# Kernel optimization log

Measured on AMD Instinct MI355X. Metric: run time of the kernel, lower is better.

The kernel has to match this reference:

```python
import jax, jax.numpy as jnp
import numpy as np

K_HOPS = 10
ALPHA = 0.1


def setup_inputs() -> dict:
    key = jax.random.key(0)
    ks = jax.random.split(key, 12)
    B, H, N, IC, F, C = 4096, 5, 30, 256, 512, 4
    real = jax.random.normal(ks[0], (B, N, IC), jnp.float32)
    imag = jax.random.normal(ks[1], (B, N, IC), jnp.float32)
    graph = jax.random.normal(ks[2], (B, H, N, N), jnp.float32)
    def lin(k, fan_in, shape):
        s = 1.0 / np.sqrt(fan_in)
        return jax.random.uniform(k, shape, jnp.float32, -s, s)
    W1 = lin(ks[3], IC, (IC, F)); b1 = lin(ks[4], IC, (F,))
    W2 = lin(ks[5], F, (F, F));  b2 = lin(ks[6], F, (F,))
    Wl = lin(ks[7], F, (F, 1));  bl = lin(ks[8], F, (1,))
    Wc = lin(ks[9], N, (C, N));  bc = lin(ks[10], N, (C,))
    return {"real": real, "imag": imag, "graph": graph,
            "W1": W1, "b1": b1, "W2": W2, "b2": b2,
            "Wl": Wl, "bl": bl, "Wc": Wc, "bc": bc}


def _appnp(S, x):
    # x_{k+1} = alpha * x0 + (1 - alpha) * S @ x_k, K iterations
    x0 = x
    def step(h, _):
        h = ALPHA * x0 + (1.0 - ALPHA) * jnp.einsum('bij,bjf->bif', S, h)
        return h, None
    h, _ = jax.lax.scan(step, x, None, length=K_HOPS)
    return h


def _prop_matrix(graph):
    # adj = mean over frequency dim; edges = nonzero entries (weights discarded
    # by the original code), self loops added, symmetric gcn_norm with
    # degree = column sums; source->target flow => operator is transposed.
    adj = jnp.mean(graph, axis=1)                      # [B,N,N]
    M = (adj != 0).astype(graph.dtype)
    N = M.shape[-1]
    Mt = M + jnp.eye(N, dtype=graph.dtype)             # add self loops
    deg = jnp.sum(Mt, axis=-2)                         # in-degree (col sums) [B,N]
    dinv = jax.lax.rsqrt(deg)
    S = dinv[:, :, None] * jnp.swapaxes(Mt, -1, -2) * dinv[:, None, :]
    return S


def reference(real, imag, graph, W1, b1, W2, b2, Wl, bl, Wc, bc):
    S = _prop_matrix(graph)
    # layer 1: linear -> relu -> APPNP(K=10)
    x = jax.nn.relu(jnp.einsum('bni,if->bnf', real, W1) + b1)
    x = _appnp(S, x)
    # layer 2: linear -> relu -> APPNP(K=10)
    x = jax.nn.relu(jnp.einsum('bnf,fg->bng', x, W2) + b2)
    x = _appnp(S, x)
    # readout: per-node linear to scalar, relu, then Conv1d(30->C, k=1)
    x = jax.nn.relu(jnp.einsum('bnf,fo->bno', x, Wl)[..., 0] + bl[0])  # [B,N]
    out = jnp.einsum('bn,cn->bc', x, Wc) + bc                          # [B,C]
    return out
```

## Files before the change

kernel.cpp:

```cpp
#include <hip/hip_runtime.h>
#include <hip/hip_bf16.h>

typedef _Float16 f16;
typedef _Float16 f16x8 __attribute__((ext_vector_type(8)));
typedef _Float16 f16x4 __attribute__((ext_vector_type(4)));
typedef float f32x4 __attribute__((ext_vector_type(4)));

#define P_OFF   0
#define W1T_OFF 14745600
#define W2T_OFF 15007744

__global__ __launch_bounds__(256) void k_prop(const float* __restrict__ graph,
                                              float* __restrict__ P,
                                              const float* __restrict__ W1,
                                              const float* __restrict__ W2,
                                              f16* __restrict__ w1t,
                                              f16* __restrict__ w2t) {
    __shared__ float MtS[4][990];
    __shared__ float dinvS[4][32];
    __shared__ f16 qhS[4][1024];
    __shared__ f16 qlS[4][1024];

    if (blockIdx.x >= 1024) {
        long base = ((long)(blockIdx.x - 1024) * 256 + threadIdx.x) * 8;
        #pragma unroll
        for (int j = 0; j < 8; ++j) {
            long id = base + j;
            if (id < 131072) {
                int f = (int)(id >> 8), k = (int)(id & 255);
                w1t[id] = (f16)W1[k * 512 + f];
            } else {
                long i = id - 131072;
                int f = (int)(i >> 9), k = (int)(i & 511);
                w2t[i] = (f16)W2[k * 512 + f];
            }
        }
        return;
    }

    const int wv = threadIdx.x >> 6, lane = threadIdx.x & 63;
    const int lr = lane & 15, gq = lane >> 4;
    const long b = (long)blockIdx.x * 4 + wv;
    const float* g = graph + b * 4500;
    float* Mt = MtS[wv];
    float* dinv = dinvS[wv];
    f16* qh = qhS[wv];
    f16* ql = qlS[wv];

    for (int rep = 0; rep < 15; ++rep) {
        int e = rep * 64 + lane;
        if (e < 900) {
            float s = g[e] + g[900 + e] + g[1800 + e] + g[2700 + e] + g[3600 + e];
            int r = e / 30, c = e - r * 30;
            Mt[r * 33 + c] = ((s != 0.f) ? 1.f : 0.f) + ((r == c) ? 1.f : 0.f);
        }
    }
    __syncthreads();
    if (lane < 30) {
        float d = 0.f;
        #pragma unroll
        for (int r = 0; r < 30; ++r) d += Mt[r * 33 + lane];
        dinv[lane] = 1.0f / sqrtf(d);
    }
    __syncthreads();

    auto Sval = [&](int i, int j) -> float {
        if (i >= 30 || j >= 30) return 0.f;
        return dinv[i] * Mt[j * 33 + i] * dinv[j];
    };

    f16x8 sh[2], sl[2];
    #pragma unroll
    for (int mi = 0; mi < 2; ++mi)
        #pragma unroll
        for (int jj = 0; jj < 8; ++jj) {
            float v = Sval(mi * 16 + lr, gq * 8 + jj);
            f16 h = (f16)v;
            sh[mi][jj] = h;
            sl[mi][jj] = (f16)(v - (float)h);
        }

    f32x4 qd[2][2], racc[2][2];
    #pragma unroll
    for (int mi = 0; mi < 2; ++mi)
        #pragma unroll
        for (int ni = 0; ni < 2; ++ni)
            #pragma unroll
            for (int r = 0; r < 4; ++r) {
                int row = mi * 16 + gq * 4 + r, col = ni * 16 + lr;
                qd[mi][ni][r] = Sval(row, col);
                racc[mi][ni][r] = (row == col) ? 0.1f : 0.f;
            }

    float c = 0.1f;
    for (int k = 1; k <= 9; ++k) {
        c *= 0.9f;
        #pragma unroll
        for (int mi = 0; mi < 2; ++mi)
            #pragma unroll
            for (int ni = 0; ni < 2; ++ni) {
                racc[mi][ni] += c * qd[mi][ni];
                f16x4 hh, ll;
                #pragma unroll
                for (int r = 0; r < 4; ++r) {
                    float v = qd[mi][ni][r];
                    f16 h = (f16)v;
                    hh[r] = h;
                    ll[r] = (f16)(v - (float)h);
                }
                const int col = ni * 16 + lr, rowb = mi * 16 + gq * 4;
                *reinterpret_cast<f16x4*>(qh + col * 32 + rowb) = hh;
                *reinterpret_cast<f16x4*>(ql + col * 32 + rowb) = ll;
            }
        __syncthreads();
        f16x8 bh[2], bl[2];
        #pragma unroll
        for (int ni = 0; ni < 2; ++ni) {
            const int col = ni * 16 + lr;
            bh[ni] = *reinterpret_cast<const f16x8*>(qh + col * 32 + gq * 8);
            bl[ni] = *reinterpret_cast<const f16x8*>(ql + col * 32 + gq * 8);
        }
        #pragma unroll
        for (int mi = 0; mi < 2; ++mi)
            #pragma unroll
            for (int ni = 0; ni < 2; ++ni) {
                f32x4 d = {0.f, 0.f, 0.f, 0.f};
                d = __builtin_amdgcn_mfma_f32_16x16x32_f16(sh[mi], bh[ni], d, 0, 0, 0);
                d = __builtin_amdgcn_mfma_f32_16x16x32_f16(sh[mi], bl[ni], d, 0, 0, 0);
                d = __builtin_amdgcn_mfma_f32_16x16x32_f16(sl[mi], bh[ni], d, 0, 0, 0);
                qd[mi][ni] = d;
            }
        __syncthreads();
    }
    const float cf = 0.3486784401f;
    #pragma unroll
    for (int mi = 0; mi < 2; ++mi)
        #pragma unroll
        for (int ni = 0; ni < 2; ++ni)
            #pragma unroll
            for (int r = 0; r < 4; ++r) {
                int row = mi * 16 + gq * 4 + r, col = ni * 16 + lr;
                if (row < 30 && col < 30)
                    P[b * 900 + row * 30 + col] = racc[mi][ni][r] + cf * qd[mi][ni][r];
            }
}

#define SMEM_BYTES 152576
#define PF_OFF   131072
#define B1L_OFF  141312
#define B2L_OFF  143360
#define WLL_OFF  145408
#define RED_OFF  147456
#define VL_OFF   151552
#define ZL_OFF   152064

__global__ __launch_bounds__(512, 2) void k_main(
    const float* __restrict__ real, const f16* __restrict__ w1t,
    const f16* __restrict__ w2t, const float* __restrict__ b1,
    const float* __restrict__ b2, const float* __restrict__ wl,
    const float* __restrict__ bl, const float* __restrict__ wc,
    const float* __restrict__ bc, const float* __restrict__ Pws,
    float* __restrict__ out) {
    extern __shared__ char smem[];
    char*  buf = smem;
    f16*   Pf  = (f16*)(smem + PF_OFF);
    float* b1l = (float*)(smem + B1L_OFF);
    float* b2l = (float*)(smem + B2L_OFF);
    float* wll = (float*)(smem + WLL_OFF);
    float* red = (float*)(smem + RED_OFF);
    float* vl  = (float*)(smem + VL_OFF);
    float* zl  = (float*)(smem + ZL_OFF);

    const int tid  = threadIdx.x;
    const int lane = tid & 63;
    const int wv   = tid >> 6;
    const int gq   = lane >> 4;
    const int lr   = lane & 15;
    const int blk  = blockIdx.x;
    const long r0  = (long)blk * 120;

    {
        const int srow = tid >> 2;
        const int seg  = tid & 3;
        const int rr   = srow & 31;
        const bool valid = rr < 30;
        const float* p = real + (r0 + (long)(srow >> 5) * 30 + rr) * 256 + seg * 64;
        #pragma unroll
        for (int q = 0; q < 8; ++q) {
            f32x4 v0 = {0.f,0.f,0.f,0.f}, v1 = {0.f,0.f,0.f,0.f};
            if (valid) {
                v0 = *reinterpret_cast<const f32x4*>(p + q * 8);
                v1 = *reinterpret_cast<const f32x4*>(p + q * 8 + 4);
            }
            f16x8 h;
            h[0]=(f16)v0[0]; h[1]=(f16)v0[1]; h[2]=(f16)v0[2]; h[3]=(f16)v0[3];
            h[4]=(f16)v1[0]; h[5]=(f16)v1[1]; h[6]=(f16)v1[2]; h[7]=(f16)v1[3];
            *reinterpret_cast<f16x8*>(
                buf + srow * 512 + ((seg * 128 + q * 16) ^ ((srow & 7) << 4))) = h;
        }
    }
    #pragma unroll
    for (int s = 0; s < 8; ++s) {
        int e = tid + s * 512;
        int bb = e >> 10, idx = e & 1023, n = idx >> 5, kk = idx & 31;
        float p = (n < 30 && kk < 30)
            ? Pws[((long)blk * 4 + bb) * 900 + n * 30 + kk] : 0.f;
        Pf[bb * 1280 + n * 40 + kk] = (f16)p;
    }
    b1l[tid] = b1[tid];
    b2l[tid] = b2[tid];
    wll[tid] = wl[tid];

    f32x4 acc[4][8];
    #pragma unroll
    for (int a = 0; a < 4; ++a)
        #pragma unroll
        for (int b = 0; b < 8; ++b) { f32x4 z = {0.f,0.f,0.f,0.f}; acc[a][b] = z; }
    __syncthreads();

    const f16* w1p = w1t + (wv * 64 + lr) * 256;
    {
        f16x8 waA[4], waB[4];
        #pragma unroll
        for (int mi = 0; mi < 4; ++mi) {
            waA[mi] = *reinterpret_cast<const f16x8*>(w1p + mi * 4096 + gq * 8);
            waB[mi] = *reinterpret_cast<const f16x8*>(w1p + mi * 4096 + 32 + gq * 8);
        }
        #pragma unroll
        for (int kc2 = 0; kc2 < 4; ++kc2) {
            #pragma unroll
            for (int half = 0; half < 2; ++half) {
                const int kc = 2 * kc2 + half;
                f16x8 bf[8];
                #pragma unroll
                for (int ni = 0; ni < 8; ++ni) {
                    const int row = ni * 16 + lr;
                    bf[ni] = *reinterpret_cast<const f16x8*>(
                        buf + row * 512 + ((kc * 64 + gq * 16) ^ ((row & 7) << 4)));
                }
                __builtin_amdgcn_s_setprio(1);
                #pragma unroll
                for (int mi = 0; mi < 4; ++mi)
                    #pragma unroll
                    for (int ni = 0; ni < 8; ++ni)
                        acc[mi][ni] = __builtin_amdgcn_mfma_f32_16x16x32_f16(
                            half ? waB[mi] : waA[mi], bf[ni], acc[mi][ni], 0, 0, 0);
                __builtin_amdgcn_s_setprio(0);
                if (kc + 2 < 8) {
                    #pragma unroll
                    for (int mi = 0; mi < 4; ++mi) {
                        f16x8 w = *reinterpret_cast<const f16x8*>(
                            w1p + mi * 4096 + (kc + 2) * 32 + gq * 8);
                        if (half) waB[mi] = w; else waA[mi] = w;
                    }
                }
            }
        }
    }
    __syncthreads();

    #pragma unroll
    for (int mi = 0; mi < 4; ++mi) {
        const int featb = wv * 64 + mi * 16 + gq * 4;
        float b1v[4];
        #pragma unroll
        for (int j = 0; j < 4; ++j) b1v[j] = b1l[featb + j];
        #pragma unroll
        for (int ni = 0; ni < 8; ++ni) {
            const int node = ni * 16 + lr;
            f16x4 h;
            #pragma unroll
            for (int j = 0; j < 4; ++j)
                h[j] = (f16)fmaxf(acc[mi][ni][j] + b1v[j], 0.f);
            *reinterpret_cast<f16x4*>(
                buf + node * 1024 + ((featb * 2) ^ ((node & 15) << 4))) = h;
        }
    }
    #pragma unroll
    for (int a = 0; a < 4; ++a)
        #pragma unroll
        for (int b = 0; b < 8; ++b) { f32x4 z = {0.f,0.f,0.f,0.f}; acc[a][b] = z; }
    __syncthreads();

    const f16* w2p = w2t + (wv * 64 + lr) * 512;
    {
        f16x8 bfA[4], bfB[4];
        #pragma unroll
        for (int ni = 0; ni < 4; ++ni) {
            bfA[ni] = *reinterpret_cast<const f16x8*>(w2p + ni * 8192 + gq * 8);
            bfB[ni] = *reinterpret_cast<const f16x8*>(w2p + ni * 8192 + 32 + gq * 8);
        }
        #pragma unroll
        for (int kc2 = 0; kc2 < 8; ++kc2) {
            #pragma unroll
            for (int half = 0; half < 2; ++half) {
                const int kc = 2 * kc2 + half;
                f16x8 af[8];
                #pragma unroll
                for (int mi = 0; mi < 8; ++mi) {
                    const int row = mi * 16 + lr;
                    af[mi] = *reinterpret_cast<const f16x8*>(
                        buf + row * 1024 + (((kc * 32 + gq * 8) * 2) ^ ((row & 15) << 4)));
                }
                __builtin_amdgcn_s_setprio(1);
                #pragma unroll
                for (int mi = 0; mi < 8; ++mi)
                    #pragma unroll
                    for (int ni = 0; ni < 4; ++ni)
                        acc[ni][mi] = __builtin_amdgcn_mfma_f32_16x16x32_f16(
                            af[mi], half ? bfB[ni] : bfA[ni], acc[ni][mi], 0, 0, 0);
                __builtin_amdgcn_s_setprio(0);
                if (kc + 2 < 16) {
                    #pragma unroll
                    for (int ni = 0; ni < 4; ++ni) {
                        f16x8 w = *reinterpret_cast<const f16x8*>(
                            w2p + ni * 8192 + (kc + 2) * 32 + gq * 8);
                        if (half) bfB[ni] = w; else bfA[ni] = w;
                    }
                }
            }
        }
    }
    __syncthreads();

    #pragma unroll
    for (int mi = 0; mi < 8; ++mi)
        #pragma unroll
        for (int ni = 0; ni < 4; ++ni) {
            const int feat  = wv * 64 + ni * 16 + lr;
            const int node0 = mi * 16 + gq * 4;
            f16x4 h;
            #pragma unroll
            for (int j = 0; j < 4; ++j) h[j] = (f16)acc[ni][mi][j];
            *reinterpret_cast<f16x4*>(
                buf + feat * 256 + ((node0 * 2) ^ ((feat & 15) << 4))) = h;
        }
    __syncthreads();

    {
        f16x8 pb[4][2];
        #pragma unroll
        for (int bb = 0; bb < 4; ++bb)
            #pragma unroll
            for (int ni = 0; ni < 2; ++ni)
                pb[bb][ni] = *reinterpret_cast<const f16x8*>(
                    Pf + bb * 1280 + (ni * 16 + lr) * 40 + gq * 8);
        float vacc[4][2];
        #pragma unroll
        for (int bb = 0; bb < 4; ++bb)
            #pragma unroll
            for (int ni = 0; ni < 2; ++ni) vacc[bb][ni] = 0.f;
        #pragma unroll
        for (int mi = 0; mi < 4; ++mi) {
            const int featb = wv * 64 + mi * 16;
            float b2v[4], wlv[4];
            #pragma unroll
            for (int j = 0; j < 4; ++j) {
                b2v[j] = b2l[featb + gq * 4 + j];
                wlv[j] = wll[featb + gq * 4 + j];
            }
            f16x8 au[4];
            #pragma unroll
            for (int bb = 0; bb < 4; ++bb) {
                const int feat = featb + lr;
                au[bb] = *reinterpret_cast<const f16x8*>(
                    buf + feat * 256 + ((bb * 64 + gq * 16) ^ ((feat & 15) << 4)));
            }
            #pragma unroll
            for (int bb = 0; bb < 4; ++bb)
                #pragma unroll
                for (int ni = 0; ni < 2; ++ni) {
                    f32x4 d = {0.f,0.f,0.f,0.f};
                    d = __builtin_amdgcn_mfma_f32_16x16x32_f16(au[bb], pb[bb][ni], d, 0, 0, 0);
                    #pragma unroll
                    for (int j = 0; j < 4; ++j) {
                        float y = fmaxf(d[j] + b2v[j], 0.f);
                        vacc[bb][ni] = fmaf(y, wlv[j], vacc[bb][ni]);
                    }
                }
        }
        #pragma unroll
        for (int bb = 0; bb < 4; ++bb)
            #pragma unroll
            for (int ni = 0; ni < 2; ++ni) {
                float v = vacc[bb][ni];
                v += __shfl_xor(v, 16);
                v += __shfl_xor(v, 32);
                if (lane < 16) red[wv * 128 + bb * 32 + ni * 16 + lr] = v;
            }
    }
    __syncthreads();
    if (tid < 128) {
        float s = 0.f;
        #pragma unroll
        for (int w = 0; w < 8; ++w) s += red[w * 128 + tid];
        vl[tid] = s;
    }
    __syncthreads();
    if (tid < 120) {
        const int bb = tid / 30, n = tid - bb * 30;
        const float* Pr = Pws + ((long)blk * 4 + bb) * 900 + n * 30;
        float z = bl[0];
        #pragma unroll
        for (int j = 0; j < 30; ++j) z = fmaf(Pr[j], vl[bb * 32 + j], z);
        zl[tid] = fmaxf(z, 0.f);
    }
    __syncthreads();
    if (tid < 16) {
        const int bb = tid >> 2, cc = tid & 3;
        float o = bc[cc];
        #pragma unroll
        for (int n = 0; n < 30; ++n) o = fmaf(zl[bb * 30 + n], wc[cc * 30 + n], o);
        out[((long)blk * 4 + bb) * 4 + cc] = o;
    }
}

extern "C" void kernel_launch(void* const* d_in, const int* in_sizes, int n_in,
                              void* d_out, int out_size, void* d_ws, size_t ws_size,
                              hipStream_t stream) {
    const float* real  = (const float*)d_in[0];
    const float* graph = (const float*)d_in[2];
    const float* W1    = (const float*)d_in[3];
    const float* b1    = (const float*)d_in[4];
    const float* W2    = (const float*)d_in[5];
    const float* b2    = (const float*)d_in[6];
    const float* Wl    = (const float*)d_in[7];
    const float* bl    = (const float*)d_in[8];
    const float* Wc    = (const float*)d_in[9];
    const float* bc    = (const float*)d_in[10];
    float* out = (float*)d_out;
    char*  ws  = (char*)d_ws;

    float* Pws = (float*)(ws + P_OFF);
    f16*   w1t = (f16*)(ws + W1T_OFF);
    f16*   w2t = (f16*)(ws + W2T_OFF);

    k_prop<<<1216, 256, 0, stream>>>(graph, Pws, W1, W2, w1t, w2t);
    (void)hipFuncSetAttribute((const void*)k_main,
                              hipFuncAttributeMaxDynamicSharedMemorySize, SMEM_BYTES);
    k_main<<<1024, 512, SMEM_BYTES, stream>>>(real, w1t, w2t, b1, b2, Wl, bl, Wc, bc,
                                              Pws, out);
}
```

Before: 184.5 us.

## Halve main-kernel block to two graphs per 256-thread workgroup

The main kernel now processes 2 graphs (60 nodes) per block with 4 waves instead of 4 graphs with 8 waves, and launches twice as many blocks. Each wave covers 128 features instead of 64, so the per-wave tiles become 8x4 MFMA tiles and weight fragments are reused across fewer node tiles. Shared memory per block roughly halves, which lets more blocks fit per CU and spreads work over more blocks. In exchange, the weight matrices are read from global memory twice as often in total, and each wave holds more weight registers.

```diff
diff --git a/kernel.cpp b/kernel.cpp
--- a/kernel.cpp
+++ b/kernel.cpp
@@ -145,16 +145,16 @@
             }
 }
 
-#define SMEM_BYTES 152576
-#define PF_OFF   131072
-#define B1L_OFF  141312
-#define B2L_OFF  143360
-#define WLL_OFF  145408
-#define RED_OFF  147456
-#define VL_OFF   151552
-#define ZL_OFF   152064
-
-__global__ __launch_bounds__(512, 2) void k_main(
+#define SMEM_BYTES 78336
+#define PF_OFF   65536
+#define B1L_OFF  70656
+#define B2L_OFF  72704
+#define WLL_OFF  74752
+#define RED_OFF  76800
+#define VL_OFF   77824
+#define ZL_OFF   78080
+
+__global__ __launch_bounds__(256, 2) void k_main(
     const float* __restrict__ real, const f16* __restrict__ w1t,
     const f16* __restrict__ w2t, const float* __restrict__ b1,
     const float* __restrict__ b2, const float* __restrict__ wl,
@@ -177,7 +177,7 @@
     const int gq   = lane >> 4;
     const int lr   = lane & 15;
     const int blk  = blockIdx.x;
-    const long r0  = (long)blk * 120;
+    const long r0  = (long)blk * 60;
 
     {
         const int srow = tid >> 2;
@@ -201,28 +201,28 @@
     }
     #pragma unroll
     for (int s = 0; s < 8; ++s) {
-        int e = tid + s * 512;
+        int e = tid + s * 256;
         int bb = e >> 10, idx = e & 1023, n = idx >> 5, kk = idx & 31;
         float p = (n < 30 && kk < 30)
-            ? Pws[((long)blk * 4 + bb) * 900 + n * 30 + kk] : 0.f;
+            ? Pws[((long)blk * 2 + bb) * 900 + n * 30 + kk] : 0.f;
         Pf[bb * 1280 + n * 40 + kk] = (f16)p;
     }
-    b1l[tid] = b1[tid];
-    b2l[tid] = b2[tid];
-    wll[tid] = wl[tid];
-
-    f32x4 acc[4][8];
-    #pragma unroll
-    for (int a = 0; a < 4; ++a)
-        #pragma unroll
-        for (int b = 0; b < 8; ++b) { f32x4 z = {0.f,0.f,0.f,0.f}; acc[a][b] = z; }
-    __syncthreads();
-
-    const f16* w1p = w1t + (wv * 64 + lr) * 256;
+    b1l[tid] = b1[tid];         b1l[tid + 256] = b1[tid + 256];
+    b2l[tid] = b2[tid];         b2l[tid + 256] = b2[tid + 256];
+    wll[tid] = wl[tid];         wll[tid + 256] = wl[tid + 256];
+
+    f32x4 acc[8][4];
+    #pragma unroll
+    for (int a = 0; a < 8; ++a)
+        #pragma unroll
+        for (int b = 0; b < 4; ++b) { f32x4 z = {0.f,0.f,0.f,0.f}; acc[a][b] = z; }
+    __syncthreads();
+
+    const f16* w1p = w1t + (wv * 128 + lr) * 256;
     {
-        f16x8 waA[4], waB[4];
-        #pragma unroll
-        for (int mi = 0; mi < 4; ++mi) {
+        f16x8 waA[8], waB[8];
+        #pragma unroll
+        for (int mi = 0; mi < 8; ++mi) {
             waA[mi] = *reinterpret_cast<const f16x8*>(w1p + mi * 4096 + gq * 8);
             waB[mi] = *reinterpret_cast<const f16x8*>(w1p + mi * 4096 + 32 + gq * 8);
         }
@@ -231,24 +231,24 @@
             #pragma unroll
             for (int half = 0; half < 2; ++half) {
                 const int kc = 2 * kc2 + half;
-                f16x8 bf[8];
-                #pragma unroll
-                for (int ni = 0; ni < 8; ++ni) {
+                f16x8 bf[4];
+                #pragma unroll
+                for (int ni = 0; ni < 4; ++ni) {
                     const int row = ni * 16 + lr;
                     bf[ni] = *reinterpret_cast<const f16x8*>(
                         buf + row * 512 + ((kc * 64 + gq * 16) ^ ((row & 7) << 4)));
                 }
                 __builtin_amdgcn_s_setprio(1);
                 #pragma unroll
-                for (int mi = 0; mi < 4; ++mi)
+                for (int mi = 0; mi < 8; ++mi)
                     #pragma unroll
-                    for (int ni = 0; ni < 8; ++ni)
+                    for (int ni = 0; ni < 4; ++ni)
                         acc[mi][ni] = __builtin_amdgcn_mfma_f32_16x16x32_f16(
                             half ? waB[mi] : waA[mi], bf[ni], acc[mi][ni], 0, 0, 0);
                 __builtin_amdgcn_s_setprio(0);
                 if (kc + 2 < 8) {
                     #pragma unroll
-                    for (int mi = 0; mi < 4; ++mi) {
+                    for (int mi = 0; mi < 8; ++mi) {
                         f16x8 w = *reinterpret_cast<const f16x8*>(
                             w1p + mi * 4096 + (kc + 2) * 32 + gq * 8);
                         if (half) waB[mi] = w; else waA[mi] = w;
@@ -260,13 +260,13 @@
     __syncthreads();
 
     #pragma unroll
-    for (int mi = 0; mi < 4; ++mi) {
-        const int featb = wv * 64 + mi * 16 + gq * 4;
+    for (int mi = 0; mi < 8; ++mi) {
+        const int featb = wv * 128 + mi * 16 + gq * 4;
         float b1v[4];
         #pragma unroll
         for (int j = 0; j < 4; ++j) b1v[j] = b1l[featb + j];
         #pragma unroll
-        for (int ni = 0; ni < 8; ++ni) {
+        for (int ni = 0; ni < 4; ++ni) {
             const int node = ni * 16 + lr;
             f16x4 h;
             #pragma unroll
@@ -277,45 +277,45 @@
         }
     }
     #pragma unroll
-    for (int a = 0; a < 4; ++a)
-        #pragma unroll
-        for (int b = 0; b < 8; ++b) { f32x4 z = {0.f,0.f,0.f,0.f}; acc[a][b] = z; }
-    __syncthreads();
-
-    const f16* w2p = w2t + (wv * 64 + lr) * 512;
+    for (int a = 0; a < 8; ++a)
+        #pragma unroll
+        for (int b = 0; b < 4; ++b) { f32x4 z = {0.f,0.f,0.f,0.f}; acc[a][b] = z; }
+    __syncthreads();
+
+    const f16* w2p = w2t + (wv * 128 + lr) * 512;
     {
-        f16x8 bfA[4], bfB[4];
-        #pragma unroll
-        for (int ni = 0; ni < 4; ++ni) {
-            bfA[ni] = *reinterpret_cast<const f16x8*>(w2p + ni * 8192 + gq * 8);
-            bfB[ni] = *reinterpret_cast<const f16x8*>(w2p + ni * 8192 + 32 + gq * 8);
+        f16x8 bwA[8], bwB[8];
+        #pragma unroll
+        for (int fi = 0; fi < 8; ++fi) {
+            bwA[fi] = *reinterpret_cast<const f16x8*>(w2p + fi * 8192 + gq * 8);
+            bwB[fi] = *reinterpret_cast<const f16x8*>(w2p + fi * 8192 + 32 + gq * 8);
         }
         #pragma unroll
         for (int kc2 = 0; kc2 < 8; ++kc2) {
             #pragma unroll
             for (int half = 0; half < 2; ++half) {
                 const int kc = 2 * kc2 + half;
-                f16x8 af[8];
-                #pragma unroll
-                for (int mi = 0; mi < 8; ++mi) {
-                    const int row = mi * 16 + lr;
-                    af[mi] = *reinterpret_cast<const f16x8*>(
+                f16x8 af[4];
+                #pragma unroll
+                for (int nj = 0; nj < 4; ++nj) {
+                    const int row = nj * 16 + lr;
+                    af[nj] = *reinterpret_cast<const f16x8*>(
                         buf + row * 1024 + (((kc * 32 + gq * 8) * 2) ^ ((row & 15) << 4)));
                 }
                 __builtin_amdgcn_s_setprio(1);
                 #pragma unroll
-                for (int mi = 0; mi < 8; ++mi)
+                for (int fi = 0; fi < 8; ++fi)
                     #pragma unroll
-                    for (int ni = 0; ni < 4; ++ni)
-                        acc[ni][mi] = __builtin_amdgcn_mfma_f32_16x16x32_f16(
-                            af[mi], half ? bfB[ni] : bfA[ni], acc[ni][mi], 0, 0, 0);
+                    for (int nj = 0; nj < 4; ++nj)
+                        acc[fi][nj] = __builtin_amdgcn_mfma_f32_16x16x32_f16(
+                            af[nj], half ? bwB[fi] : bwA[fi], acc[fi][nj], 0, 0, 0);
                 __builtin_amdgcn_s_setprio(0);
                 if (kc + 2 < 16) {
                     #pragma unroll
-                    for (int ni = 0; ni < 4; ++ni) {
+                    for (int fi = 0; fi < 8; ++fi) {
                         f16x8 w = *reinterpret_cast<const f16x8*>(
-                            w2p + ni * 8192 + (kc + 2) * 32 + gq * 8);
-                        if (half) bfB[ni] = w; else bfA[ni] = w;
+                            w2p + fi * 8192 + (kc + 2) * 32 + gq * 8);
+                        if (half) bwB[fi] = w; else bwA[fi] = w;
                     }
                 }
             }
@@ -324,50 +324,50 @@
     __syncthreads();
 
     #pragma unroll
-    for (int mi = 0; mi < 8; ++mi)
-        #pragma unroll
-        for (int ni = 0; ni < 4; ++ni) {
-            const int feat  = wv * 64 + ni * 16 + lr;
-            const int node0 = mi * 16 + gq * 4;
+    for (int fi = 0; fi < 8; ++fi)
+        #pragma unroll
+        for (int nj = 0; nj < 4; ++nj) {
+            const int feat  = wv * 128 + fi * 16 + lr;
+            const int node0 = nj * 16 + gq * 4;
             f16x4 h;
             #pragma unroll
-            for (int j = 0; j < 4; ++j) h[j] = (f16)acc[ni][mi][j];
+            for (int j = 0; j < 4; ++j) h[j] = (f16)acc[fi][nj][j];
             *reinterpret_cast<f16x4*>(
-                buf + feat * 256 + ((node0 * 2) ^ ((feat & 15) << 4))) = h;
+                buf + feat * 128 + ((node0 * 2) ^ ((feat & 7) << 4))) = h;
         }
     __syncthreads();
 
     {
-        f16x8 pb[4][2];
-        #pragma unroll
-        for (int bb = 0; bb < 4; ++bb)
+        f16x8 pb[2][2];
+        #pragma unroll
+        for (int bb = 0; bb < 2; ++bb)
             #pragma unroll
             for (int ni = 0; ni < 2; ++ni)
                 pb[bb][ni] = *reinterpret_cast<const f16x8*>(
                     Pf + bb * 1280 + (ni * 16 + lr) * 40 + gq * 8);
-        float vacc[4][2];
-        #pragma unroll
-        for (int bb = 0; bb < 4; ++bb)
+        float vacc[2][2];
+        #pragma unroll
+        for (int bb = 0; bb < 2; ++bb)
             #pragma unroll
             for (int ni = 0; ni < 2; ++ni) vacc[bb][ni] = 0.f;
         #pragma unroll
-        for (int mi = 0; mi < 4; ++mi) {
-            const int featb = wv * 64 + mi * 16;
+        for (int mi = 0; mi < 8; ++mi) {
+            const int featb = wv * 128 + mi * 16;
             float b2v[4], wlv[4];
             #pragma unroll
             for (int j = 0; j < 4; ++j) {
                 b2v[j] = b2l[featb + gq * 4 + j];
                 wlv[j] = wll[featb + gq * 4 + j];
             }
-            f16x8 au[4];
-            #pragma unroll
-            for (int bb = 0; bb < 4; ++bb) {
+            f16x8 au[2];
+            #pragma unroll
+            for (int bb = 0; bb < 2; ++bb) {
                 const int feat = featb + lr;
                 au[bb] = *reinterpret_cast<const f16x8*>(
-                    buf + feat * 256 + ((bb * 64 + gq * 16) ^ ((feat & 15) << 4)));
-            }
-            #pragma unroll
-            for (int bb = 0; bb < 4; ++bb)
+                    buf + feat * 128 + ((bb * 64 + gq * 16) ^ ((feat & 7) << 4)));
+            }
+            #pragma unroll
+            for (int bb = 0; bb < 2; ++bb)
                 #pragma unroll
                 for (int ni = 0; ni < 2; ++ni) {
                     f32x4 d = {0.f,0.f,0.f,0.f};
@@ -380,38 +380,38 @@
                 }
         }
         #pragma unroll
-        for (int bb = 0; bb < 4; ++bb)
+        for (int bb = 0; bb < 2; ++bb)
             #pragma unroll
             for (int ni = 0; ni < 2; ++ni) {
                 float v = vacc[bb][ni];
                 v += __shfl_xor(v, 16);
                 v += __shfl_xor(v, 32);
-                if (lane < 16) red[wv * 128 + bb * 32 + ni * 16 + lr] = v;
-            }
-    }
-    __syncthreads();
-    if (tid < 128) {
+                if (lane < 16) red[wv * 64 + bb * 32 + ni * 16 + lr] = v;
+            }
+    }
+    __syncthreads();
+    if (tid < 64) {
         float s = 0.f;
         #pragma unroll
-        for (int w = 0; w < 8; ++w) s += red[w * 128 + tid];
+        for (int w = 0; w < 4; ++w) s += red[w * 64 + tid];
         vl[tid] = s;
     }
     __syncthreads();
-    if (tid < 120) {
+    if (tid < 60) {
         const int bb = tid / 30, n = tid - bb * 30;
-        const float* Pr = Pws + ((long)blk * 4 + bb) * 900 + n * 30;
+        const float* Pr = Pws + ((long)blk * 2 + bb) * 900 + n * 30;
         float z = bl[0];
         #pragma unroll
         for (int j = 0; j < 30; ++j) z = fmaf(Pr[j], vl[bb * 32 + j], z);
         zl[tid] = fmaxf(z, 0.f);
     }
     __syncthreads();
-    if (tid < 16) {
+    if (tid < 8) {
         const int bb = tid >> 2, cc = tid & 3;
         float o = bc[cc];
         #pragma unroll
         for (int n = 0; n < 30; ++n) o = fmaf(zl[bb * 30 + n], wc[cc * 30 + n], o);
-        out[((long)blk * 4 + bb) * 4 + cc] = o;
+        out[((long)blk * 2 + bb) * 4 + cc] = o;
     }
 }
 
@@ -438,6 +438,6 @@
     k_prop<<<1216, 256, 0, stream>>>(graph, Pws, W1, W2, w1t, w2t);
     (void)hipFuncSetAttribute((const void*)k_main,
                               hipFuncAttributeMaxDynamicSharedMemorySize, SMEM_BYTES);
-    k_main<<<1024, 512, SMEM_BYTES, stream>>>(real, w1t, w2t, b1, b2, Wl, bl, Wc, bc,
+    k_main<<<2048, 256, SMEM_BYTES, stream>>>(real, w1t, w2t, b1, b2, Wl, bl, Wc, bc,
                                               Pws, out);
 }
```

New measurement: 253.3 us. 1.37x slower.

## Fuse propagation-matrix computation into main kernel with warp specialization

Applied to the files above, without the earlier changes.

Moves the per-graph propagation matrix computation (adjacency, normalization, power-series of S via MFMA) from a separate kernel into k_main. Four waves compute P directly into shared memory while the other four load and convert the input rows, and the prep kernel now only transposes weights. This removes the P round trip through global memory and the extra per-block prop launch work. The trade-offs are that only half the waves now load inputs, and the P computation sits on the critical path before the GEMMs. Barriers inside the P loop are replaced by per-wave lgkmcnt fences. P is still written to the workspace.

```diff
diff --git a/kernel.cpp b/kernel.cpp
--- a/kernel.cpp
+++ b/kernel.cpp
@@ -6,143 +6,32 @@
 typedef _Float16 f16x4 __attribute__((ext_vector_type(4)));
 typedef float f32x4 __attribute__((ext_vector_type(4)));
 
+#define LGKM_FENCE() do { \
+    asm volatile("s_waitcnt lgkmcnt(0)" ::: "memory"); \
+    __builtin_amdgcn_sched_barrier(0); \
+} while (0)
+
 #define P_OFF   0
 #define W1T_OFF 14745600
 #define W2T_OFF 15007744
 
-__global__ __launch_bounds__(256) void k_prop(const float* __restrict__ graph,
-                                              float* __restrict__ P,
-                                              const float* __restrict__ W1,
+__global__ __launch_bounds__(256) void k_prep(const float* __restrict__ W1,
                                               const float* __restrict__ W2,
                                               f16* __restrict__ w1t,
                                               f16* __restrict__ w2t) {
-    __shared__ float MtS[4][990];
-    __shared__ float dinvS[4][32];
-    __shared__ f16 qhS[4][1024];
-    __shared__ f16 qlS[4][1024];
-
-    if (blockIdx.x >= 1024) {
-        long base = ((long)(blockIdx.x - 1024) * 256 + threadIdx.x) * 8;
-        #pragma unroll
-        for (int j = 0; j < 8; ++j) {
-            long id = base + j;
-            if (id < 131072) {
-                int f = (int)(id >> 8), k = (int)(id & 255);
-                w1t[id] = (f16)W1[k * 512 + f];
-            } else {
-                long i = id - 131072;
-                int f = (int)(i >> 9), k = (int)(i & 511);
-                w2t[i] = (f16)W2[k * 512 + f];
-            }
-        }
-        return;
-    }
-
-    const int wv = threadIdx.x >> 6, lane = threadIdx.x & 63;
-    const int lr = lane & 15, gq = lane >> 4;
-    const long b = (long)blockIdx.x * 4 + wv;
-    const float* g = graph + b * 4500;
-    float* Mt = MtS[wv];
-    float* dinv = dinvS[wv];
-    f16* qh = qhS[wv];
-    f16* ql = qlS[wv];
-
-    for (int rep = 0; rep < 15; ++rep) {
-        int e = rep * 64 + lane;
-        if (e < 900) {
-            float s = g[e] + g[900 + e] + g[1800 + e] + g[2700 + e] + g[3600 + e];
-            int r = e / 30, c = e - r * 30;
-            Mt[r * 33 + c] = ((s != 0.f) ? 1.f : 0.f) + ((r == c) ? 1.f : 0.f);
-        }
-    }
-    __syncthreads();
-    if (lane < 30) {
-        float d = 0.f;
-        #pragma unroll
-        for (int r = 0; r < 30; ++r) d += Mt[r * 33 + lane];
-        dinv[lane] = 1.0f / sqrtf(d);
-    }
-    __syncthreads();
-
-    auto Sval = [&](int i, int j) -> float {
-        if (i >= 30 || j >= 30) return 0.f;
-        return dinv[i] * Mt[j * 33 + i] * dinv[j];
-    };
-
-    f16x8 sh[2], sl[2];
+    long base = ((long)blockIdx.x * 256 + threadIdx.x) * 8;
     #pragma unroll
-    for (int mi = 0; mi < 2; ++mi)
-        #pragma unroll
-        for (int jj = 0; jj < 8; ++jj) {
-            float v = Sval(mi * 16 + lr, gq * 8 + jj);
-            f16 h = (f16)v;
-            sh[mi][jj] = h;
-            sl[mi][jj] = (f16)(v - (float)h);
-        }
-
-    f32x4 qd[2][2], racc[2][2];
-    #pragma unroll
-    for (int mi = 0; mi < 2; ++mi)
-        #pragma unroll
-        for (int ni = 0; ni < 2; ++ni)
-            #pragma unroll
-            for (int r = 0; r < 4; ++r) {
-                int row = mi * 16 + gq * 4 + r, col = ni * 16 + lr;
-                qd[mi][ni][r] = Sval(row, col);
-                racc[mi][ni][r] = (row == col) ? 0.1f : 0.f;
-            }
-
-    float c = 0.1f;
-    for (int k = 1; k <= 9; ++k) {
-        c *= 0.9f;
-        #pragma unroll
-        for (int mi = 0; mi < 2; ++mi)
-            #pragma unroll
-            for (int ni = 0; ni < 2; ++ni) {
-                racc[mi][ni] += c * qd[mi][ni];
-                f16x4 hh, ll;
-                #pragma unroll
-                for (int r = 0; r < 4; ++r) {
-                    float v = qd[mi][ni][r];
-                    f16 h = (f16)v;
-                    hh[r] = h;
-                    ll[r] = (f16)(v - (float)h);
-                }
-                const int col = ni * 16 + lr, rowb = mi * 16 + gq * 4;
-                *reinterpret_cast<f16x4*>(qh + col * 32 + rowb) = hh;
-                *reinterpret_cast<f16x4*>(ql + col * 32 + rowb) = ll;
-            }
-        __syncthreads();
-        f16x8 bh[2], bl[2];
-        #pragma unroll
-        for (int ni = 0; ni < 2; ++ni) {
-            const int col = ni * 16 + lr;
-            bh[ni] = *reinterpret_cast<const f16x8*>(qh + col * 32 + gq * 8);
-            bl[ni] = *reinterpret_cast<const f16x8*>(ql + col * 32 + gq * 8);
-        }
-        #pragma unroll
-        for (int mi = 0; mi < 2; ++mi)
-            #pragma unroll
-            for (int ni = 0; ni < 2; ++ni) {
-                f32x4 d = {0.f, 0.f, 0.f, 0.f};
-                d = __builtin_amdgcn_mfma_f32_16x16x32_f16(sh[mi], bh[ni], d, 0, 0, 0);
-                d = __builtin_amdgcn_mfma_f32_16x16x32_f16(sh[mi], bl[ni], d, 0, 0, 0);
-                d = __builtin_amdgcn_mfma_f32_16x16x32_f16(sl[mi], bh[ni], d, 0, 0, 0);
-                qd[mi][ni] = d;
-            }
-        __syncthreads();
-    }
-    const float cf = 0.3486784401f;
-    #pragma unroll
-    for (int mi = 0; mi < 2; ++mi)
-        #pragma unroll
-        for (int ni = 0; ni < 2; ++ni)
-            #pragma unroll
-            for (int r = 0; r < 4; ++r) {
-                int row = mi * 16 + gq * 4 + r, col = ni * 16 + lr;
-                if (row < 30 && col < 30)
-                    P[b * 900 + row * 30 + col] = racc[mi][ni][r] + cf * qd[mi][ni][r];
-            }
+    for (int j = 0; j < 8; ++j) {
+        long id = base + j;
+        if (id < 131072) {
+            int f = (int)(id >> 8), k = (int)(id & 255);
+            w1t[id] = (f16)W1[k * 512 + f];
+        } else {
+            long i = id - 131072;
+            int f = (int)(i >> 9), k = (int)(i & 511);
+            w2t[i] = (f16)W2[k * 512 + f];
+        }
+    }
 }
 
 #define SMEM_BYTES 152576
@@ -159,8 +48,8 @@
     const f16* __restrict__ w2t, const float* __restrict__ b1,
     const float* __restrict__ b2, const float* __restrict__ wl,
     const float* __restrict__ bl, const float* __restrict__ wc,
-    const float* __restrict__ bc, const float* __restrict__ Pws,
-    float* __restrict__ out) {
+    const float* __restrict__ bc, const float* __restrict__ graph,
+    float* __restrict__ Pws, float* __restrict__ out) {
     extern __shared__ char smem[];
     char*  buf = smem;
     f16*   Pf  = (f16*)(smem + PF_OFF);
@@ -179,14 +68,19 @@
     const int blk  = blockIdx.x;
     const long r0  = (long)blk * 120;
 
-    {
-        const int srow = tid >> 2;
-        const int seg  = tid & 3;
+    b1l[tid] = b1[tid];
+    b2l[tid] = b2[tid];
+    wll[tid] = wl[tid];
+
+    if (wv >= 4) {
+        const int t    = tid & 255;
+        const int srow = t >> 1;
+        const int half = t & 1;
         const int rr   = srow & 31;
         const bool valid = rr < 30;
-        const float* p = real + (r0 + (long)(srow >> 5) * 30 + rr) * 256 + seg * 64;
-        #pragma unroll
-        for (int q = 0; q < 8; ++q) {
+        const float* p = real + (r0 + (long)(srow >> 5) * 30 + rr) * 256 + half * 128;
+        #pragma unroll
+        for (int q = 0; q < 16; ++q) {
             f32x4 v0 = {0.f,0.f,0.f,0.f}, v1 = {0.f,0.f,0.f,0.f};
             if (valid) {
                 v0 = *reinterpret_cast<const f32x4*>(p + q * 8);
@@ -196,20 +90,116 @@
             h[0]=(f16)v0[0]; h[1]=(f16)v0[1]; h[2]=(f16)v0[2]; h[3]=(f16)v0[3];
             h[4]=(f16)v1[0]; h[5]=(f16)v1[1]; h[6]=(f16)v1[2]; h[7]=(f16)v1[3];
             *reinterpret_cast<f16x8*>(
-                buf + srow * 512 + ((seg * 128 + q * 16) ^ ((srow & 7) << 4))) = h;
-        }
-    }
-    #pragma unroll
-    for (int s = 0; s < 8; ++s) {
-        int e = tid + s * 512;
-        int bb = e >> 10, idx = e & 1023, n = idx >> 5, kk = idx & 31;
-        float p = (n < 30 && kk < 30)
-            ? Pws[((long)blk * 4 + bb) * 900 + n * 30 + kk] : 0.f;
-        Pf[bb * 1280 + n * 40 + kk] = (f16)p;
-    }
-    b1l[tid] = b1[tid];
-    b2l[tid] = b2[tid];
-    wll[tid] = wl[tid];
+                buf + srow * 512 + ((half * 256 + q * 16) ^ ((srow & 7) << 4))) = h;
+        }
+    } else {
+        char*  sc   = buf + 65536 + wv * 8192;
+        float* Mt   = (float*)sc;
+        float* dinv = (float*)(sc + 3968);
+        f16*   qh   = (f16*)(sc + 4096);
+        f16*   ql   = (f16*)(sc + 6144);
+        const long b = (long)blk * 4 + wv;
+        const float* g = graph + b * 4500;
+
+        #pragma unroll
+        for (int rep = 0; rep < 15; ++rep) {
+            int e = rep * 64 + lane;
+            if (e < 900) {
+                float s = g[e] + g[900 + e] + g[1800 + e] + g[2700 + e] + g[3600 + e];
+                int r = e / 30, c = e - r * 30;
+                Mt[r * 33 + c] = ((s != 0.f) ? 1.f : 0.f) + ((r == c) ? 1.f : 0.f);
+            }
+        }
+        LGKM_FENCE();
+        if (lane < 30) {
+            float d = 0.f;
+            #pragma unroll
+            for (int r = 0; r < 30; ++r) d += Mt[r * 33 + lane];
+            dinv[lane] = 1.0f / sqrtf(d);
+        }
+        LGKM_FENCE();
+
+        auto Sval = [&](int i, int j) -> float {
+            if (i >= 30 || j >= 30) return 0.f;
+            return dinv[i] * Mt[j * 33 + i] * dinv[j];
+        };
+
+        f16x8 sh[2], sl[2];
+        #pragma unroll
+        for (int mi = 0; mi < 2; ++mi)
+            #pragma unroll
+            for (int jj = 0; jj < 8; ++jj) {
+                float v = Sval(mi * 16 + lr, gq * 8 + jj);
+                f16 h = (f16)v;
+                sh[mi][jj] = h;
+                sl[mi][jj] = (f16)(v - (float)h);
+            }
+
+        f32x4 qd[2][2], racc[2][2];
+        #pragma unroll
+        for (int mi = 0; mi < 2; ++mi)
+            #pragma unroll
+            for (int ni = 0; ni < 2; ++ni)
+                #pragma unroll
+                for (int r = 0; r < 4; ++r) {
+                    int row = mi * 16 + gq * 4 + r, col = ni * 16 + lr;
+                    qd[mi][ni][r] = Sval(row, col);
+                    racc[mi][ni][r] = (row == col) ? 0.1f : 0.f;
+                }
+
+        float c = 0.1f;
+        for (int k = 1; k <= 9; ++k) {
+            c *= 0.9f;
+            #pragma unroll
+            for (int mi = 0; mi < 2; ++mi)
+                #pragma unroll
+                for (int ni = 0; ni < 2; ++ni) {
+                    racc[mi][ni] += c * qd[mi][ni];
+                    f16x4 hh, ll;
+                    #pragma unroll
+                    for (int r = 0; r < 4; ++r) {
+                        float v = qd[mi][ni][r];
+                        f16 h = (f16)v;
+                        hh[r] = h;
+                        ll[r] = (f16)(v - (float)h);
+                    }
+                    const int col = ni * 16 + lr, rowb = mi * 16 + gq * 4;
+                    *reinterpret_cast<f16x4*>(qh + col * 32 + rowb) = hh;
+                    *reinterpret_cast<f16x4*>(ql + col * 32 + rowb) = ll;
+                }
+            LGKM_FENCE();
+            f16x8 bh[2], bl2[2];
+            #pragma unroll
+            for (int ni = 0; ni < 2; ++ni) {
+                const int col = ni * 16 + lr;
+                bh[ni]  = *reinterpret_cast<const f16x8*>(qh + col * 32 + gq * 8);
+                bl2[ni] = *reinterpret_cast<const f16x8*>(ql + col * 32 + gq * 8);
+            }
+            #pragma unroll
+            for (int mi = 0; mi < 2; ++mi)
+                #pragma unroll
+                for (int ni = 0; ni < 2; ++ni) {
+                    f32x4 d = {0.f, 0.f, 0.f, 0.f};
+                    d = __builtin_amdgcn_mfma_f32_16x16x32_f16(sh[mi], bh[ni],  d, 0, 0, 0);
+                    d = __builtin_amdgcn_mfma_f32_16x16x32_f16(sh[mi], bl2[ni], d, 0, 0, 0);
+                    d = __builtin_amdgcn_mfma_f32_16x16x32_f16(sl[mi], bh[ni],  d, 0, 0, 0);
+                    qd[mi][ni] = d;
+                }
+        }
+        const float cf = 0.3486784401f;
+        #pragma unroll
+        for (int mi = 0; mi < 2; ++mi)
+            #pragma unroll
+            for (int ni = 0; ni < 2; ++ni)
+                #pragma unroll
+                for (int r = 0; r < 4; ++r) {
+                    int row = mi * 16 + gq * 4 + r, col = ni * 16 + lr;
+                    float val = racc[mi][ni][r] + cf * qd[mi][ni][r];
+                    bool in = (row < 30 && col < 30);
+                    Pf[wv * 1280 + row * 40 + col] = (f16)(in ? val : 0.f);
+                    if (in) Pws[b * 900 + row * 30 + col] = val;
+                }
+    }
 
     f32x4 acc[4][8];
     #pragma unroll
@@ -435,9 +425,9 @@
     f16*   w1t = (f16*)(ws + W1T_OFF);
     f16*   w2t = (f16*)(ws + W2T_OFF);
 
-    k_prop<<<1216, 256, 0, stream>>>(graph, Pws, W1, W2, w1t, w2t);
+    k_prep<<<192, 256, 0, stream>>>(W1, W2, w1t, w2t);
     (void)hipFuncSetAttribute((const void*)k_main,
                               hipFuncAttributeMaxDynamicSharedMemorySize, SMEM_BYTES);
     k_main<<<1024, 512, SMEM_BYTES, stream>>>(real, w1t, w2t, b1, b2, Wl, bl, Wc, bc,
-                                              Pws, out);
+                                              graph, Pws, out);
 }
```

Result: faster. 172.4 us (-6.5%).
